# Kernel optimization log

Measured on AMD Instinct MI355X. Metric: run time of the kernel, lower is better.

## Reference

```python
import jax, jax.numpy as jnp
import numpy as np

N = 6144      # total nodes
G = 32        # graphs
NPG = 192     # nodes per graph (N = G*NPG)
FIN = 32      # num_node_features
FE = 8        # num_edge_features
H = 64        # layers = [64, 64]
HM = 128      # layers_MLP = [128]
C = 2         # num_classes
K = 8         # opts.knn
E = 49152     # given edges
EPS = 1e-5


def _bn(x, g, b):
    # BatchNorm1d in train mode: biased batch stats
    m = x.mean(0)
    v = x.var(0)
    return (x - m) * jax.lax.rsqrt(v + EPS) * g + b


def setup_inputs() -> dict:
    key = jax.random.key(0)
    ks = jax.random.split(key, 24)

    def w(k, shape):
        return (jax.random.normal(k, shape, jnp.float32)
                * (1.0 / np.sqrt(shape[0])).astype(np.float32))

    x = jax.random.normal(ks[0], (N, FIN), jnp.float32)
    edge_index = jax.random.randint(ks[1], (2, E), 0, N)
    edge_attr = jax.random.normal(ks[2], (E, FE), jnp.float32)
    batch = jnp.arange(N, dtype=jnp.int64 if jax.config.jax_enable_x64 else jnp.int32) // NPG
    return dict(
        x=x, edge_index=edge_index, edge_attr=edge_attr, batch=batch,
        # EdgeFeatsConv layer 1: mlp(Linear(2*FIN+FE,H), ReLU, Linear(H,H)) + root weight
        ef_w1=w(ks[3], (2 * FIN + FE, H)), ef_b1=jnp.zeros((H,), jnp.float32),
        ef_w2=w(ks[4], (H, H)), ef_b2=jnp.zeros((H,), jnp.float32),
        ef_wroot=w(ks[5], (FIN, H)),
        bn1_g=jnp.ones((H,), jnp.float32), bn1_b=jnp.zeros((H,), jnp.float32),
        # EdgeConv layer 2: mlp(Linear(2*H,H), ReLU, Linear(H,H)), aggr=max
        ec_w1=w(ks[6], (2 * H, H)), ec_b1=jnp.zeros((H,), jnp.float32),
        ec_w2=w(ks[7], (H, H)), ec_b2=jnp.zeros((H,), jnp.float32),
        bn2_g=jnp.ones((H,), jnp.float32), bn2_b=jnp.zeros((H,), jnp.float32),
        # model2: Linear(H,HM), BN, ReLU, Linear(HM,C)
        m2_w1=w(ks[8], (H, HM)), m2_b1=jnp.zeros((HM,), jnp.float32),
        m2_bng=jnp.ones((HM,), jnp.float32), m2_bnb=jnp.zeros((HM,), jnp.float32),
        m2_w2=w(ks[9], (HM, C)), m2_b2=jnp.zeros((C,), jnp.float32),
    )


def reference(x, edge_index, edge_attr, batch,
              ef_w1, ef_b1, ef_w2, ef_b2, ef_wroot, bn1_g, bn1_b,
              ec_w1, ec_b1, ec_w2, ec_b2, bn2_g, bn2_b,
              m2_w1, m2_b1, m2_bng, m2_bnb, m2_w2, m2_b2):
    src, dst = edge_index[0], edge_index[1]

    # ---- layer 1: EdgeFeatsConv (edge-conditioned message MLP + root weight, aggr=sum)
    m = jnp.concatenate([x[dst], x[src], edge_attr], axis=1) @ ef_w1 + ef_b1
    m = jax.nn.relu(m) @ ef_w2 + ef_b2
    x1 = jax.ops.segment_sum(m, dst, num_segments=N) + x @ ef_wroot
    x1 = _bn(x1, bn1_g, bn1_b)

    # ---- layer 2: dynamic KNN graph (loop=False) + to_undirected, then EdgeConv (aggr=max)
    sq = jnp.sum(x1 * x1, axis=1)
    d2 = sq[:, None] + sq[None, :] - 2.0 * (x1 @ x1.T)       # [N, N]
    d2 = d2.at[jnp.arange(N), jnp.arange(N)].set(jnp.inf)    # no self loops
    _, nbr = jax.lax.top_k(-d2, K)                           # [N, K] nearest neighbors
    dst0 = jnp.repeat(jnp.arange(N), K)
    src0 = nbr.reshape(-1)
    s = jnp.concatenate([src0, dst0])                        # undirected (dups OK: max aggr)
    d = jnp.concatenate([dst0, src0])

    h = jnp.concatenate([x1[d], x1[s] - x1[d]], axis=1) @ ec_w1 + ec_b1
    h = jax.nn.relu(h) @ ec_w2 + ec_b2
    x2 = jax.ops.segment_max(h, d, num_segments=N)
    x2 = _bn(x2, bn2_g, bn2_b)

    # ---- per-graph all-pairs |g_i - g_z| (row order: for z, for i)
    g = x2.reshape(G, NPG, H)
    diff = jnp.abs(g[:, None, :, :] - g[:, :, None, :]).reshape(-1, H)  # [G*NPG*NPG, H]

    # ---- model2 MLP + log_softmax
    h2 = jax.nn.relu(_bn(diff @ m2_w1 + m2_b1, m2_bng, m2_bnb))
    out = h2 @ m2_w2 + m2_b2
    return jax.nn.log_softmax(out, axis=1)
```

## Files before the change

### kernel.cpp

```cpp
#include <hip/hip_runtime.h>

#define NN 6144
#define GG 32
#define NPGc 192
#define FINc 32
#define FEc 8
#define Hc 64
#define HMc 128
#define Kc 8
#define Ec 49152
#define NKc (NN*Kc)
#define RTOTc (GG*NPGc*NPGc)

typedef float f32x4 __attribute__((ext_vector_type(4)));
typedef short bf16x8 __attribute__((ext_vector_type(8)));
typedef unsigned long long u64;

__device__ __forceinline__ unsigned short f2bf(float f){
  unsigned u = __float_as_uint(f);
  unsigned r = u + 0x7fffu + ((u>>16)&1u);
  return (unsigned short)(r>>16);
}
__device__ __forceinline__ unsigned fenc(float f){
  unsigned u = __float_as_uint(f);
  return (u & 0x80000000u) ? ~u : (u | 0x80000000u);
}
__device__ __forceinline__ float fdec(unsigned e){
  unsigned u = (e & 0x80000000u) ? (e & 0x7fffffffu) : ~e;
  return __uint_as_float(u);
}
__device__ __forceinline__ void bub8(u64* t8, u64 k){
#pragma unroll
  for (int q=0;q<8;q++){ u64 cur=t8[q]; u64 lo=(k<cur)?k:cur; u64 hi=(k<cur)?cur:k; t8[q]=lo; k=hi; }
}

__global__ void k_init(float* dbins, float* stats){
  int idx = blockIdx.x*256 + threadIdx.x;
  if (idx < 64*256) dbins[idx] = 0.f;
  if (idx < 768) stats[idx] = 0.f;
}

__global__ __launch_bounds__(256) void k_root(const float* __restrict__ x, const float* __restrict__ wr, float* __restrict__ x1a){
  __shared__ float Ws[FINc*Hc];
  __shared__ float xr[4][FINc];
  int t = threadIdx.x;
  for (int q=t;q<FINc*Hc;q+=256) Ws[q] = wr[q];
  int rg = t>>6, j = t&63;
  int r = blockIdx.x*4 + rg;
  if (j < FINc) xr[rg][j] = x[r*FINc + j];
  __syncthreads();
  float a0=0.f, a1=0.f;
#pragma unroll
  for (int k=0;k<FINc;k+=2){
    a0 = fmaf(xr[rg][k],   Ws[k*Hc+j],     a0);
    a1 = fmaf(xr[rg][k+1], Ws[(k+1)*Hc+j], a1);
  }
  x1a[r*Hc + j] = a0 + a1;
}

__global__ __launch_bounds__(256) void k_eac(const float* __restrict__ ea, const float* __restrict__ w1, float* __restrict__ EAc){
  __shared__ float Wc[FEc*Hc];
  int t = threadIdx.x;
  for (int q=t; q<FEc*Hc; q+=256) Wc[q] = w1[64*Hc + q];
  __syncthreads();
  int idx = blockIdx.x*256 + t;
  int e = idx >> 4, c4 = (idx & 15)*4;
  float av[8];
#pragma unroll
  for (int q=0;q<8;q++) av[q] = ea[e*FEc + q];
  float4 o = {0.f,0.f,0.f,0.f};
#pragma unroll
  for (int q=0;q<8;q++){
    o.x = fmaf(av[q], Wc[q*Hc + c4+0], o.x);
    o.y = fmaf(av[q], Wc[q*Hc + c4+1], o.y);
    o.z = fmaf(av[q], Wc[q*Hc + c4+2], o.z);
    o.w = fmaf(av[q], Wc[q*Hc + c4+3], o.w);
  }
  *(float4*)(EAc + (size_t)e*Hc + c4) = o;
}

__global__ __launch_bounds__(256) void k_p12(const float* __restrict__ x, const float* __restrict__ w1, const float* __restrict__ b1,
                                             float* __restrict__ P1, float* __restrict__ P2){
  __shared__ float xs[16][32];
  int t = threadIdx.x;
  int j = t & 63, w = t >> 6;
  float wa[32], wb[32];
#pragma unroll
  for (int k=0;k<32;k++){
    wa[k] = w1[k*Hc + j];
    wb[k] = w1[(32+k)*Hc + j];
  }
  float b1j = b1[j];
  int nb = blockIdx.x * 16;
  for (int q=t; q<16*32; q+=256) xs[q>>5][q&31] = x[(size_t)(nb + (q>>5))*FINc + (q&31)];
  __syncthreads();
#pragma unroll
  for (int it=0; it<4; it++){
    int nl = it*4 + w;
    float a = b1j, b = 0.f;
#pragma unroll
    for (int k=0;k<32;k++){
      float xv = xs[nl][k];
      a = fmaf(xv, wa[k], a);
      b = fmaf(xv, wb[k], b);
    }
    int n = nb + nl;
    P1[(size_t)n*Hc + j] = a;
    P2[(size_t)n*Hc + j] = b;
  }
}

__global__ void k_zero_cnt(unsigned* rcnt){
  int idx = blockIdx.x*256 + threadIdx.x;
  if (idx < NN) rcnt[idx] = 0u;
}
__global__ void k_cnt_dst(const int* __restrict__ ei, unsigned* __restrict__ rcnt){
  int e = blockIdx.x*256 + threadIdx.x;
  atomicAdd(&rcnt[ei[Ec + e]], 1u);
}
__global__ __launch_bounds__(256) void k_scan(const unsigned* __restrict__ rcnt, unsigned* __restrict__ rptr, unsigned* __restrict__ rcur){
  __shared__ unsigned ps[256];
// ... 33 lines not shown
__global__ __launch_bounds__(128) void k_node1(const float* __restrict__ P1, const float* __restrict__ P2, const float* __restrict__ EAc,
        const int* __restrict__ ei, const unsigned* __restrict__ rptr, const unsigned* __restrict__ rlist,
        const float* __restrict__ w2, const float* __restrict__ b2, float* __restrict__ x1a){
  __shared__ __align__(16) float accs[16][68];
  __shared__ __align__(16) float W2T[64][68];
  __shared__ unsigned rp_s[17];
  int t = threadIdx.x;
  int d0 = blockIdx.x * 16;
  for (int q=t; q<64*64; q+=128) W2T[q&63][q>>6] = w2[q];
  if (t < 17) rp_s[t] = rptr[d0 + t];
  __syncthreads();
  int slot = t>>3, cg = t&7, c0 = cg*8;
  int n = d0 + slot;
  float4 p1a = *(const float4*)(P1 + (size_t)n*Hc + c0);
  float4 p1b = *(const float4*)(P1 + (size_t)n*Hc + c0 + 4);
  float acc[8];
#pragma unroll
  for (int q=0;q<8;q++) acc[q] = 0.f;
  unsigned beg = rp_s[slot], end = rp_s[slot+1];
  for (unsigned pos=beg; pos<end; pos++){
    unsigned e = rlist[pos];
    int s = ei[e];
    float4 qa = *(const float4*)(P2 + (size_t)s*Hc + c0);
    float4 qb = *(const float4*)(P2 + (size_t)s*Hc + c0 + 4);
    float4 fa = *(const float4*)(EAc + (size_t)e*Hc + c0);
    float4 fb = *(const float4*)(EAc + (size_t)e*Hc + c0 + 4);
    acc[0] += fmaxf(p1a.x + qa.x + fa.x, 0.f);
    acc[1] += fmaxf(p1a.y + qa.y + fa.y, 0.f);
    acc[2] += fmaxf(p1a.z + qa.z + fa.z, 0.f);
    acc[3] += fmaxf(p1a.w + qa.w + fa.w, 0.f);
    acc[4] += fmaxf(p1b.x + qb.x + fb.x, 0.f);
    acc[5] += fmaxf(p1b.y + qb.y + fb.y, 0.f);
    acc[6] += fmaxf(p1b.z + qb.z + fb.z, 0.f);
    acc[7] += fmaxf(p1b.w + qb.w + fb.w, 0.f);
  }
  *(float4*)&accs[slot][c0]   = make_float4(acc[0],acc[1],acc[2],acc[3]);
  *(float4*)&accs[slot][c0+4] = make_float4(acc[4],acc[5],acc[6],acc[7]);
  __syncthreads();
  float out[8];
#pragma unroll
  for (int q=0;q<8;q++) out[q] = 0.f;
  for (int k4=0;k4<16;k4++){
    float4 hv = *(const float4*)&accs[slot][k4*4];
#pragma unroll
    for (int cc=0;cc<8;cc++){
      float4 wv = *(const float4*)&W2T[c0+cc][k4*4];
      out[cc] = fmaf(hv.x,wv.x, fmaf(hv.y,wv.y, fmaf(hv.z,wv.z, fmaf(hv.w,wv.w, out[cc]))));
    }
  }
  float deg = (float)(end - beg);
  float* px = x1a + (size_t)n*Hc + c0;
#pragma unroll
  for (int cc=0;cc<8;cc++) px[cc] += out[cc] + deg*b2[c0+cc];
}

__global__ __launch_bounds__(256) void k_bn_stats(const float* __restrict__ src, float* __restrict__ gsum, float* __restrict__ gss){
  int t = threadIdx.x;
  int c = t & 63;
  int r0 = blockIdx.x*64 + (t>>6);
  float s=0.f, ss=0.f;
  for (int it=0; it<16; it++){
    int r = r0 + it*4;
    float v = src[r*Hc + c];
    s += v; ss += v*v;
  }
  __shared__ float S[64], SS[64];
  if (t < 64){ S[t]=0.f; SS[t]=0.f; }
  __syncthreads();
  atomicAdd(&S[c], s); atomicAdd(&SS[c], ss);
  __syncthreads();
  if (t < 64){ atomicAdd(&gsum[t], S[t]); atomicAdd(&gss[t], SS[t]); }
}

__global__ void k_bn_fin(const float* gsum, const float* gss, const float* gam, const float* bet, float* sc, float* sh){
  int c = threadIdx.x;
  float mean = gsum[c] / (float)NN;
  float var  = gss[c] / (float)NN - mean*mean;
  float rs = rsqrtf(var + 1e-5f);
  float s = rs * gam[c];
  sc[c] = s; sh[c] = bet[c] - mean*s;
}

__global__ __launch_bounds__(256) void k_apply_bn1_sq(const float* __restrict__ x1a, const float* __restrict__ sc, const float* __restrict__ sh,
                               float* __restrict__ x1bn, float* __restrict__ sqv){
  int t = threadIdx.x;
  int c = t & 63;
  int r = blockIdx.x*4 + (t>>6);
  float v = x1a[r*Hc + c]*sc[c] + sh[c];
  x1bn[r*Hc + c] = v;
  float s = v*v;
#pragma unroll
  for (int off=1; off<64; off<<=1) s += __shfl_xor(s, off, 64);
  if (c == 0) sqv[r] = s;
}

__global__ __launch_bounds__(128,2) void k_knn(const float* __restrict__ x1bn, const float* __restrict__ sqv, u64* __restrict__ parts, int CH){
  __shared__ __align__(16) float XJ[64][68];
  __shared__ float sqj[64];
  int t = threadIdx.x;
  int i1 = blockIdx.x*256 + t;
  int i2 = i1 + 128;
  float4 xa[16], xb[16];
#pragma unroll
  for (int q=0;q<16;q++){
    xa[q] = *(const float4*)(x1bn + (size_t)i1*Hc + q*4);
    xb[q] = *(const float4*)(x1bn + (size_t)i2*Hc + q*4);
  }
  float sqi1 = sqv[i1], sqi2 = sqv[i2];
  u64 t8a[8], t8b[8];
#pragma unroll
  for (int q=0;q<8;q++){ t8a[q] = ~0ull; t8b[q] = ~0ull; }
  float thra = __uint_as_float(0x7f800000u);
  float thrb = thra;
  int cpc = NN / CH;
  int nsub = cpc >> 6;
  int jbase0 = blockIdx.y * cpc;
  for (int sub=0; sub<nsub; sub++){
    int jb = jbase0 + sub*64;
    __syncthreads();
    {
      int c = t>>1, hh = t&1;
      const float4* srcp = (const float4*)(x1bn + (size_t)(jb + c)*Hc + hh*32);
#pragma unroll
      for (int q=0;q<8;q++) *(float4*)&XJ[c][hh*32 + q*4] = srcp[q];
      if (t < 64) sqj[t] = sqv[jb + t];
    }
    __syncthreads();
    for (int j=0;j<64;j++){
      float sqjc = sqj[j];
      float a0=0.f,a1=0.f,a2=0.f,a3=0.f,b0=0.f,b1=0.f,b2=0.f,b3=0.f;
#pragma unroll
      for (int q4=0;q4<4;q4++){
        float4 xj0 = *(const float4*)&XJ[j][q4*16];
        float4 xj1 = *(const float4*)&XJ[j][q4*16+4];
        float4 xj2 = *(const float4*)&XJ[j][q4*16+8];
        float4 xj3 = *(const float4*)&XJ[j][q4*16+12];
        float4 A0 = xa[q4*4+0], A1 = xa[q4*4+1], A2v = xa[q4*4+2], A3 = xa[q4*4+3];
        float4 B0 = xb[q4*4+0], B1 = xb[q4*4+1], B2v = xb[q4*4+2], B3 = xb[q4*4+3];
        a0=fmaf(A0.x,xj0.x,a0); a1=fmaf(A0.y,xj0.y,a1); a2=fmaf(A0.z,xj0.z,a2); a3=fmaf(A0.w,xj0.w,a3);
        b0=fmaf(B0.x,xj0.x,b0); b1=fmaf(B0.y,xj0.y,b1); b2=fmaf(B0.z,xj0.z,b2); b3=fmaf(B0.w,xj0.w,b3);
        a0=fmaf(A1.x,xj1.x,a0); a1=fmaf(A1.y,xj1.y,a1); a2=fmaf(A1.z,xj1.z,a2); a3=fmaf(A1.w,xj1.w,a3);
        b0=fmaf(B1.x,xj1.x,b0); b1=fmaf(B1.y,xj1.y,b1); b2=fmaf(B1.z,xj1.z,b2); b3=fmaf(B1.w,xj1.w,b3);
        a0=fmaf(A2v.x,xj2.x,a0); a1=fmaf(A2v.y,xj2.y,a1); a2=fmaf(A2v.z,xj2.z,a2); a3=fmaf(A2v.w,xj2.w,a3);
        b0=fmaf(B2v.x,xj2.x,b0); b1=fmaf(B2v.y,xj2.y,b1); b2=fmaf(B2v.z,xj2.z,b2); b3=fmaf(B2v.w,xj2.w,b3);
        a0=fmaf(A3.x,xj3.x,a0); a1=fmaf(A3.y,xj3.y,a1); a2=fmaf(A3.z,xj3.z,a2); a3=fmaf(A3.w,xj3.w,a3);
        b0=fmaf(B3.x,xj3.x,b0); b1=fmaf(B3.y,xj3.y,b1); b2=fmaf(B3.z,xj3.z,b2); b3=fmaf(B3.w,xj3.w,b3);
      }
      float dot1 = (a0+a1)+(a2+a3);
      float dot2 = (b0+b1)+(b2+b3);
      int jj = jb + j;
      float d2a = (sqi1 + sqjc) - 2.f*dot1;
      float d2b = (sqi2 + sqjc) - 2.f*dot2;
      bool ia = !(d2a > thra) && (jj != i1);
      bool ib = !(d2b > thrb) && (jj != i2);
      if (__builtin_expect(ia | ib, 0)){
        if (ia){
          u64 ka = (((u64)fenc(d2a))<<32) | (unsigned)jj;
          bub8(t8a, ka);
          thra = fdec((unsigned)(t8a[7]>>32));
        }
        if (ib){
          u64 kb = (((u64)fenc(d2b))<<32) | (unsigned)jj;
          bub8(t8b, kb);
          thrb = fdec((unsigned)(t8b[7]>>32));
        }
      }
    }
  }
  u64* pa = parts + ((size_t)blockIdx.y*NN + i1)*8;
  u64* pb = parts + ((size_t)blockIdx.y*NN + i2)*8;
#pragma unroll
  for (int q=0;q<8;q++){ pa[q] = t8a[q]; pb[q] = t8b[q]; }
}

__global__ __launch_bounds__(256) void k_knn_merge(const u64* __restrict__ parts, int CH, unsigned* __restrict__ nbr){
  int r = blockIdx.x*256 + threadIdx.x;
  u64 t8[8];
#pragma unroll
  for (int q=0;q<8;q++) t8[q] = ~0ull;
  for (int ch=0; ch<CH; ch++){
    const u64* p = parts + ((size_t)ch*NN + r)*8;
    u64 k[8];
#pragma unroll
    for (int q=0;q<8;q++) k[q] = p[q];
#pragma unroll
    for (int q=0;q<8;q++){
      if (k[q] >= t8[7]) break;
      bub8(t8, k[q]);
    }
  }
#pragma unroll
  for (int s=0;s<8;s++) nbr[r*Kc + s] = (unsigned)(t8[s] & 0xffffffffu);
}

__global__ __launch_bounds__(256) void k_pq(const float* __restrict__ x1bn, const float* __restrict__ w1, const float* __restrict__ b1,
                                            float* __restrict__ A2, float* __restrict__ Qm){
  __shared__ float xs[16][64];
  int t = threadIdx.x;
  int j = t & 63, w = t >> 6;
  float wa[64], wb[64];
#pragma unroll
  for (int k=0;k<64;k++){
    float wt  = w1[k*64 + j];
    float wbv = w1[(64+k)*64 + j];
    wa[k] = wt - wbv; wb[k] = wbv;
  }
  float b1j = b1[j];
  int nb = blockIdx.x * 16;
  for (int q=t; q<16*64; q+=256) xs[q>>6][q&63] = x1bn[(size_t)(nb + (q>>6))*64 + (q&63)];
  __syncthreads();
#pragma unroll
  for (int it=0; it<4; it++){
    int nl = it*4 + w;
    float a = b1j, qq = 0.f;
#pragma unroll
    for (int k=0;k<64;k++){
      float xv = xs[nl][k];
      a  = fmaf(xv, wa[k], a);
      qq = fmaf(xv, wb[k], qq);
    }
    int n = nb + nl;
    A2[(size_t)n*64 + j] = a;
    Qm[(size_t)n*64 + j] = qq;
  }
}

__global__ __launch_bounds__(128) void k_edge2max(const float* __restrict__ A2, const float* __restrict__ Qm,
        const unsigned* __restrict__ nbr, const unsigned* __restrict__ rptr, const unsigned* __restrict__ rlist,
        const float* __restrict__ w2, const float* __restrict__ b2, float* __restrict__ x2f){
  __shared__ __align__(16) float W2T[64][68];
  __shared__ __align__(16) float hidT[64][132];
  __shared__ unsigned x2s[17][64];
  __shared__ unsigned rp_s[17];
  __shared__ int wslot[128];
  int t = threadIdx.x;
  int d0 = blockIdx.x * 16;
  for (int q=t; q<64*64; q+=128) W2T[q&63][q>>6] = w2[q];
  for (int q=t; q<17*64; q+=128) ((unsigned*)x2s)[q] = 0x007FFFFFu;
  if (t < 17) rp_s[t] = rptr[d0 + t];
  __syncthreads();
  unsigned rp0 = rp_s[0];
  int total_rev = (int)(rp_s[16] - rp0);
  int eg = t & 15, cg = t >> 4;
  int r0 = eg*8, c0 = cg*8;
  float b2v[8];
#pragma unroll
  for (int cc=0;cc<8;cc++) b2v[cc] = b2[c0+cc];
  int ntile = 1 + ((total_rev + 127) >> 7);
  for (int tile=0; tile<ntile; tile++){
    int d, s, active;
    if (tile == 0){
      d = d0 + (t>>3); s = (int)nbr[(size_t)d*8 + (t&7)]; active = 1; wslot[t] = t>>3;
    } else {
      int idx = (tile-1)*128 + t;
      active = idx < total_rev;
// ... 3 lines not shown
#pragma unroll
        for (int m=1; m<16; m++) sl += (pos >= rp_s[m]) ? 1 : 0;
        s = (int)rlist[pos];
        d = d0 + sl;
        wslot[t] = sl;
      } else { d = d0; s = 0; wslot[t] = 16; }
    }
    if (active){
      const float* pa = A2 + (size_t)d*64;
      const float* pq = Qm + (size_t)s*64;
#pragma unroll
      for (int c4=0; c4<16; c4++){
        float4 va = *(const float4*)(pa + c4*4);
        float4 vq = *(const float4*)(pq + c4*4);
        hidT[c4*4+0][t] = fmaxf(va.x+vq.x, 0.f);
        hidT[c4*4+1][t] = fmaxf(va.y+vq.y, 0.f);
        hidT[c4*4+2][t] = fmaxf(va.z+vq.z, 0.f);
        hidT[c4*4+3][t] = fmaxf(va.w+vq.w, 0.f);
      }
    } else {
#pragma unroll
      for (int c4=0; c4<16; c4++){
        hidT[c4*4+0][t] = 0.f; hidT[c4*4+1][t] = 0.f;
        hidT[c4*4+2][t] = 0.f; hidT[c4*4+3][t] = 0.f;
      }
    }
    __syncthreads();
    float acc[8][8];
#pragma unroll
    for (int i=0;i<8;i++)
#pragma unroll
      for (int cc=0;cc<8;cc++) acc[i][cc] = 0.f;
    for (int k=0;k<64;k+=4){
      float4 wv[8];
#pragma unroll
      for (int cc=0;cc<8;cc++) wv[cc] = *(const float4*)&W2T[c0+cc][k];
#pragma unroll
      for (int kk=0;kk<4;kk++){
        float4 h0 = *(const float4*)&hidT[k+kk][r0];
        float4 h1 = *(const float4*)&hidT[k+kk][r0+4];
        float hh[8] = {h0.x,h0.y,h0.z,h0.w,h1.x,h1.y,h1.z,h1.w};
#pragma unroll
        for (int i=0;i<8;i++)
#pragma unroll
          for (int cc=0;cc<8;cc++)
            acc[i][cc] = fmaf(hh[i], ((const float*)&wv[cc])[kk], acc[i][cc]);
      }
    }
    int cur = wslot[r0];
    float mx[8];
#pragma unroll
    for (int cc=0;cc<8;cc++) mx[cc] = acc[0][cc];
    for (int i=1;i<8;i++){
      int sl = wslot[r0+i];
      if (sl != cur){
#pragma unroll
        for (int cc=0;cc<8;cc++) atomicMax(&x2s[cur][c0+cc], fenc(mx[cc] + b2v[cc]));
        cur = sl;
#pragma unroll
        for (int cc=0;cc<8;cc++) mx[cc] = acc[i][cc];
      } else {
#pragma unroll
        for (int cc=0;cc<8;cc++) mx[cc] = fmaxf(mx[cc], acc[i][cc]);
      }
    }
#pragma unroll
    for (int cc=0;cc<8;cc++) atomicMax(&x2s[cur][c0+cc], fenc(mx[cc] + b2v[cc]));
    __syncthreads();
  }
#pragma unroll
  for (int q=0;q<8;q++){
    int idx = t + q*128;
    int sl = idx >> 6, c = idx & 63;
    x2f[(size_t)(d0+sl)*64 + c] = fdec(x2s[sl][c]);
  }
}

__global__ __launch_bounds__(256) void k_apply_bn2f(const float* __restrict__ x2f, const float* __restrict__ sc, const float* __restrict__ sh, float* __restrict__ x2bn){
  int idx = blockIdx.x*256 + threadIdx.x;
  int c = idx & 63;
  x2bn[idx] = x2f[idx]*sc[c] + sh[c];
}

__global__ __launch_bounds__(256,2) void k_d_stats(const float* __restrict__ x2bn, const float* __restrict__ w1, float* __restrict__ dbins){
  __shared__ __align__(16) char sm[24576 + 16384 + 1024];
  unsigned char* A = (unsigned char*)sm;
  unsigned char* W = (unsigned char*)sm + 24576;
  float* Ssum = (float*)(sm + 40960);
  int t = threadIdx.x;
  int gid = blockIdx.x; int g = gid / NPGc; int z = gid - g*NPGc;
  const float* xg = x2bn + (size_t)g*NPGc*Hc;
  const float* xz = xg + z*Hc;
  Ssum[t] = 0.f;
#pragma unroll
  for (int q=0;q<8;q++){
    int task = t + 256*q; int c = task & 127; int c4 = task >> 7;
    ushort4 p;
    p.x = f2bf(w1[(4*c4+0)*HMc + c]);
    p.y = f2bf(w1[(4*c4+1)*HMc + c]);
    p.z = f2bf(w1[(4*c4+2)*HMc + c]);
    p.w = f2bf(w1[(4*c4+3)*HMc + c]);
    *(ushort4*)(W + c*128 + ((c4*8) ^ ((c&7)<<4))) = p;
  }
#pragma unroll
  for (int q=0;q<12;q++){
    int task = t + 256*q; int i = task >> 4; int c = task & 15;
    float4 a = *(const float4*)(xg + i*Hc + c*4);
    float4 b = *(const float4*)(xz + c*4);
    ushort4 p;
    p.x = f2bf(fabsf(a.x-b.x)); p.y = f2bf(fabsf(a.y-b.y));
    p.z = f2bf(fabsf(a.z-b.z)); p.w = f2bf(fabsf(a.w-b.w));
    *(ushort4*)(A + i*128 + ((c*8) ^ ((i&7)<<4))) = p;
  }
  __syncthreads();
  int w = t>>6, l = t&63, lr = l&15, lg = l>>4;
  int sw = (lr&7)<<4;
  f32x4 zero = {0.f,0.f,0.f,0.f};
  f32x4 acc[3][8];
#pragma unroll
  for (int r=0;r<3;r++)
#pragma unroll
    for (int c=0;c<8;c++) acc[r][c] = zero;
#pragma unroll
  for (int kk=0;kk<2;kk++){
    bf16x8 af[3], bfr[8];
#pragma unroll
    for (int r=0;r<3;r++){
      int row = (w*3+r)*16 + lr;
      af[r] = *(const bf16x8*)(A + row*128 + ((lg*16 + 64*kk) ^ sw));
    }
#pragma unroll
    for (int c=0;c<8;c++){
      int col = c*16 + lr;
      bfr[c] = *(const bf16x8*)(W + col*128 + ((lg*16 + 64*kk) ^ sw));
    }
#pragma unroll
    for (int r=0;r<3;r++)
#pragma unroll
      for (int c=0;c<8;c++)
        acc[r][c] = __builtin_amdgcn_mfma_f32_16x16x32_bf16(af[r], bfr[c], acc[r][c], 0,0,0);
  }
#pragma unroll
  for (int c=0;c<8;c++){
    int col = c*16 + lr;
    float s=0.f, ss=0.f;
#pragma unroll
    for (int r=0;r<3;r++)
#pragma unroll
      for (int q=0;q<4;q++){ float v = acc[r][c][q]; s += v; ss = fmaf(v,v,ss); }
    s  += __shfl_xor(s, 16, 64);  ss += __shfl_xor(ss, 16, 64);
    s  += __shfl_xor(s, 32, 64);  ss += __shfl_xor(ss, 32, 64);
    if (lg == 0){
      atomicAdd(&Ssum[col], s);
      atomicAdd(&Ssum[128+col], ss);
    }
  }
  __syncthreads();
  if (t < 128){
    int bin = gid & 63;
    atomicAdd(&dbins[bin*256 + t], Ssum[t]);
    atomicAdd(&dbins[bin*256 + 128 + t], Ssum[128+t]);
  }
}

__global__ void k_d_fin(const float* __restrict__ dbins, const float* gam, const float* bet, float* dsc, float* dsh){
  int c = threadIdx.x;
  float s=0.f, ss=0.f;
#pragma unroll 8
  for (int b=0;b<64;b++){ s += dbins[b*256 + c]; ss += dbins[b*256 + 128 + c]; }
  float mean = s / (float)RTOTc;
  float var  = ss / (float)RTOTc - mean*mean;
  float rs = rsqrtf(var + 1e-5f);
  float k = rs * gam[c];
  dsc[c] = k; dsh[c] = bet[c] - mean*k;
}

__global__ __launch_bounds__(256,2) void k_d_main(const float* __restrict__ x2bn, const float* __restrict__ w1,
                         const float* __restrict__ w2, const float* __restrict__ b2g,
                         const float* __restrict__ dsc, const float* __restrict__ dsh, float* __restrict__ out){
  __shared__ __align__(16) char sm[49152 + 4096 + 1024];
  unsigned char* A   = (unsigned char*)sm;
  unsigned char* W   = (unsigned char*)sm + 24576;
  unsigned char* W2T = (unsigned char*)sm + 49152;
  float* sS = (float*)(sm + 53248);
  int t = threadIdx.x;
  int gid = blockIdx.x; int g = gid / NPGc; int z = gid - g*NPGc;
  const float* xg = x2bn + (size_t)g*NPGc*Hc;
  const float* xz = xg + z*Hc;
  if (t < 128){ sS[t] = dsc[t]; sS[128+t] = dsh[t]; }
  {
    int c = t>>4, kc = t&15;
    ushort4 p0 = make_ushort4(0,0,0,0), p1 = make_ushort4(0,0,0,0);
    if (c < 2){
      p0.x = f2bf(w2[(kc*8+0)*2 + c]); p0.y = f2bf(w2[(kc*8+1)*2 + c]);
      p0.z = f2bf(w2[(kc*8+2)*2 + c]); p0.w = f2bf(w2[(kc*8+3)*2 + c]);
      p1.x = f2bf(w2[(kc*8+4)*2 + c]); p1.y = f2bf(w2[(kc*8+5)*2 + c]);
      p1.z = f2bf(w2[(kc*8+6)*2 + c]); p1.w = f2bf(w2[(kc*8+7)*2 + c]);
    }
    int byte = c*256 + ((kc*16) ^ ((c&7)<<4));
    *(ushort4*)(W2T + byte) = p0;
    *(ushort4*)(W2T + byte + 8) = p1;
  }
#pragma unroll
  for (int q=0;q<8;q++){
    int task = t + 256*q; int c = task & 127; int c4 = task >> 7;
    ushort4 p;
    p.x = f2bf(w1[(4*c4+0)*HMc + c]);
    p.y = f2bf(w1[(4*c4+1)*HMc + c]);
    p.z = f2bf(w1[(4*c4+2)*HMc + c]);
    p.w = f2bf(w1[(4*c4+3)*HMc + c]);
    *(ushort4*)(W + c*128 + ((c4*8) ^ ((c&7)<<4))) = p;
  }
#pragma unroll
  for (int q=0;q<12;q++){
    int task = t + 256*q; int i = task >> 4; int c = task & 15;
    float4 a = *(const float4*)(xg + i*Hc + c*4);
    float4 b = *(const float4*)(xz + c*4);
    ushort4 p;
    p.x = f2bf(fabsf(a.x-b.x)); p.y = f2bf(fabsf(a.y-b.y));
    p.z = f2bf(fabsf(a.z-b.z)); p.w = f2bf(fabsf(a.w-b.w));
    *(ushort4*)(A + i*128 + ((c*8) ^ ((i&7)<<4))) = p;
  }
  __syncthreads();
  int w = t>>6, l = t&63, lr = l&15, lg = l>>4;
  int sw = (lr&7)<<4;
  f32x4 zero = {0.f,0.f,0.f,0.f};
  f32x4 acc[3][8];
#pragma unroll
  for (int r=0;r<3;r++)
#pragma unroll
    for (int c=0;c<8;c++) acc[r][c] = zero;
#pragma unroll
  for (int kk=0;kk<2;kk++){
    bf16x8 af[3], bfr[8];
#pragma unroll
    for (int r=0;r<3;r++){
      int row = (w*3+r)*16 + lr;
      af[r] = *(const bf16x8*)(A + row*128 + ((lg*16 + 64*kk) ^ sw));
    }
#pragma unroll
    for (int c=0;c<8;c++){
      int col = c*16 + lr;
      bfr[c] = *(const bf16x8*)(W + col*128 + ((lg*16 + 64*kk) ^ sw));
    }
#pragma unroll
    for (int r=0;r<3;r++)
#pragma unroll
      for (int c=0;c<8;c++)
        acc[r][c] = __builtin_amdgcn_mfma_f32_16x16x32_bf16(af[r], bfr[c], acc[r][c], 0,0,0);
  }
  __syncthreads();
#pragma unroll
  for (int r=0;r<3;r++){
#pragma unroll
    for (int c=0;c<8;c++){
      int col = c*16 + lr;
      float scl = sS[col], shf = sS[128+col];
#pragma unroll
      for (int q=0;q<4;q++){
        int row = (w*3+r)*16 + lg*4 + q;
        float v = fmaxf(acc[r][c][q]*scl + shf, 0.f);
        *(unsigned short*)(A + row*256 + ((col*2) ^ ((row&7)<<4))) = f2bf(v);
      }
    }
  }
  __syncthreads();
  f32x4 acc2[3];
#pragma unroll
  for (int r=0;r<3;r++) acc2[r] = zero;
#pragma unroll
  for (int kk=0;kk<4;kk++){
    bf16x8 bw = *(const bf16x8*)(W2T + lr*256 + ((lg*16 + 64*kk) ^ sw));
#pragma unroll
    for (int r=0;r<3;r++){
      int row = (w*3+r)*16 + lr;
      bf16x8 ah = *(const bf16x8*)(A + row*256 + ((lg*16 + 64*kk) ^ sw));
      acc2[r] = __builtin_amdgcn_mfma_f32_16x16x32_bf16(ah, bw, acc2[r], 0,0,0);
    }
  }
  float b2a = b2g[0], b2b = b2g[1];
  size_t obase = (size_t)gid * NPGc;
#pragma unroll
  for (int r=0;r<3;r++){
#pragma unroll
    for (int q=0;q<4;q++){
      float o = acc2[r][q];
      float oo = __shfl_xor(o, 1, 64);
      if (lr < 2){
        int row = (w*3+r)*16 + lg*4 + q;
        float self = o + ((lr==0) ? b2a : b2b);
        float oth  = oo + ((lr==0) ? b2b : b2a);
        float mx = fmaxf(self, oth);
        float lse = mx + logf(expf(self-mx) + expf(oth-mx));
        out[(obase + row)*2 + lr] = self - lse;
      }
    }
  }
}

extern "C" void kernel_launch(void* const* d_in, const int* in_sizes, int n_in,
                              void* d_out, int out_size, void* d_ws, size_t ws_size,
                              hipStream_t stream){
  const float* x    = (const float*)d_in[0];
  const int*   ei   = (const int*)d_in[1];
  const float* ea   = (const float*)d_in[2];
  const float* efw1 = (const float*)d_in[4];
  const float* efb1 = (const float*)d_in[5];
  const float* efw2 = (const float*)d_in[6];
  const float* efb2 = (const float*)d_in[7];
  const float* efwr = (const float*)d_in[8];
  const float* bn1g = (const float*)d_in[9];
  const float* bn1b = (const float*)d_in[10];
  const float* ecw1 = (const float*)d_in[11];
  const float* ecb1 = (const float*)d_in[12];
  const float* ecw2 = (const float*)d_in[13];
  const float* ecb2 = (const float*)d_in[14];
  const float* bn2g = (const float*)d_in[15];
  const float* bn2b = (const float*)d_in[16];
  const float* m2w1 = (const float*)d_in[17];
  const float* m2bng = (const float*)d_in[19];
  const float* m2bnb = (const float*)d_in[20];
  const float* m2w2  = (const float*)d_in[21];
  const float* m2b2  = (const float*)d_in[22];

  char* ws = (char*)d_ws;
  float*    x1a   = (float*)(ws + 0);
  float*    x1bn  = (float*)(ws + 1572864);
  float*    x2bn  = (float*)(ws + 3145728);
  float*    x2f   = (float*)(ws + 4718592);
  float*    sqv   = (float*)(ws + 6291456);
  unsigned* nbr   = (unsigned*)(ws + 6316032);
  float*    stats = (float*)(ws + 6512640);
  float*    dbins = (float*)(ws + 6515712);
  u64*      parts = (u64*)(ws + 6581248);
  float*    A2    = (float*)(ws + 0);
  float*    Qm    = (float*)(ws + 3145728);
  float*    P1    = (float*)(ws + 3145728);
  float*    P2    = (float*)(ws + 4718592);
  unsigned* rcnt  = (unsigned*)(ws + 6581248);
  unsigned* rptr  = rcnt + 6400;
  unsigned* rcur  = rptr + 6400;
  unsigned* rlist = rcur + 6400;
  float*    EAc   = (float*)(ws + 6581248 + 4194304);
  float *g1sum = stats,     *g1ss = stats+64,  *sc1 = stats+128, *sh1 = stats+192;
  float *g2sum = stats+256, *g2ss = stats+320, *sc2 = stats+384, *sh2 = stats+448;
  float *dsc = stats+512, *dsh = stats+640;
  float* outp = (float*)d_out;

  int CH = 96;
  if (ws_size < 6581248ull + (size_t)NN*96*64) CH = 48;
  if (ws_size < 6581248ull + (size_t)NN*48*64) CH = 24;

  k_init<<<64,256,0,stream>>>(dbins, stats);
  k_root<<<1536,256,0,stream>>>(x, efwr, x1a);
  k_eac<<<3072,256,0,stream>>>(ea, efw1, EAc);
  k_zero_cnt<<<24,256,0,stream>>>(rcnt);
  k_cnt_dst<<<192,256,0,stream>>>(ei, rcnt);
  k_scan<<<1,256,0,stream>>>(rcnt, rptr, rcur);
  k_fill_dst<<<192,256,0,stream>>>(ei, rcur, rlist);
  k_p12<<<384,256,0,stream>>>(x, efw1, efb1, P1, P2);
  k_node1<<<384,128,0,stream>>>(P1, P2, EAc, ei, rptr, rlist, efw2, efb2, x1a);
  k_bn_stats<<<96,256,0,stream>>>(x1a, g1sum, g1ss);
  k_bn_fin<<<1,64,0,stream>>>(g1sum, g1ss, bn1g, bn1b, sc1, sh1);
  k_apply_bn1_sq<<<1536,256,0,stream>>>(x1a, sc1, sh1, x1bn, sqv);
  dim3 kg(24, CH);
  k_knn<<<kg,128,0,stream>>>(x1bn, sqv, parts, CH);
  k_knn_merge<<<24,256,0,stream>>>(parts, CH, nbr);
  k_zero_cnt<<<24,256,0,stream>>>(rcnt);
  k_rev_cnt<<<192,256,0,stream>>>(nbr, rcnt);
  k_scan<<<1,256,0,stream>>>(rcnt, rptr, rcur);
  k_rev_fill<<<192,256,0,stream>>>(nbr, rcur, rlist);
  k_pq<<<384,256,0,stream>>>(x1bn, ecw1, ecb1, A2, Qm);
  k_edge2max<<<384,128,0,stream>>>(A2, Qm, nbr, rptr, rlist, ecw2, ecb2, x2f);
  k_bn_stats<<<96,256,0,stream>>>(x2f, g2sum, g2ss);
  k_bn_fin<<<1,64,0,stream>>>(g2sum, g2ss, bn2g, bn2b, sc2, sh2);
  k_apply_bn2f<<<1536,256,0,stream>>>(x2f, sc2, sh2, x2bn);
  k_d_stats<<<6144,256,0,stream>>>(x2bn, m2w1, dbins);
  k_d_fin<<<1,128,0,stream>>>(dbins, m2bng, m2bnb, dsc, dsh);
  k_d_main<<<6144,256,0,stream>>>(x2bn, m2w1, m2w2, m2b2, dsc, dsh, outp);
}
```

Baseline: 554.1 us.

## Compute KNN distances with bf16x3 split MFMA instead of scalar FP32 FMAs

Replaces the scalar FP32 pairwise-dot KNN kernel with a tiled MFMA kernel. Each feature is split into three bf16 terms (hi, lo, lo2), and six cross-product pairs are laid out along a 384-wide K dimension to approximate FP32 dot products on matrix cores. Distances are staged through LDS for the per-row top-8 bubble insert. The workspace layout is changed to hold the expanded operands, and the column-chunk count is reworked. The split-bf16 precision could reorder near-tie neighbors.

```diff
diff --git a/kernel.cpp b/kernel.cpp
--- a/kernel.cpp
+++ b/kernel.cpp
@@ -11,6 +11,7 @@
 #define Ec 49152
 #define NKc (NN*Kc)
 #define RTOTc (GG*NPGc*NPGc)
+#define KEc 384
 
 typedef float f32x4 __attribute__((ext_vector_type(4)));
 typedef short bf16x8 __attribute__((ext_vector_type(8)));
@@ -236,95 +237,132 @@
 }
 
 __global__ __launch_bounds__(256) void k_apply_bn1_sq(const float* __restrict__ x1a, const float* __restrict__ sc, const float* __restrict__ sh,
-                               float* __restrict__ x1bn, float* __restrict__ sqv){
+                               float* __restrict__ x1bn, float* __restrict__ sqv,
+                               unsigned short* __restrict__ XAe, unsigned short* __restrict__ XBe){
   int t = threadIdx.x;
   int c = t & 63;
   int r = blockIdx.x*4 + (t>>6);
   float v = x1a[r*Hc + c]*sc[c] + sh[c];
   x1bn[r*Hc + c] = v;
+  unsigned short hu = f2bf(v);
+  float hf = __uint_as_float(((unsigned)hu)<<16);
+  float r1 = v - hf;
+  unsigned short lu = f2bf(r1);
+  float lf = __uint_as_float(((unsigned)lu)<<16);
+  unsigned short l2u = f2bf(r1 - lf);
+  size_t base = (size_t)r*KEc + c;
+  XAe[base      ] = hu;  XAe[base+ 64] = lu;  XAe[base+128] = l2u;
+  XAe[base+192] = hu;   XAe[base+256] = lu;  XAe[base+320] = hu;
+  XBe[base      ] = hu;  XBe[base+ 64] = hu;  XBe[base+128] = hu;
+  XBe[base+192] = lu;   XBe[base+256] = lu;  XBe[base+320] = l2u;
   float s = v*v;
 #pragma unroll
   for (int off=1; off<64; off<<=1) s += __shfl_xor(s, off, 64);
   if (c == 0) sqv[r] = s;
 }
 
-__global__ __launch_bounds__(128,2) void k_knn(const float* __restrict__ x1bn, const float* __restrict__ sqv, u64* __restrict__ parts, int CH){
-  __shared__ __align__(16) float XJ[64][68];
-  __shared__ float sqj[64];
-  int t = threadIdx.x;
-  int i1 = blockIdx.x*256 + t;
-  int i2 = i1 + 128;
-  float4 xa[16], xb[16];
-#pragma unroll
-  for (int q=0;q<16;q++){
-    xa[q] = *(const float4*)(x1bn + (size_t)i1*Hc + q*4);
-    xb[q] = *(const float4*)(x1bn + (size_t)i2*Hc + q*4);
-  }
-  float sqi1 = sqv[i1], sqi2 = sqv[i2];
-  u64 t8a[8], t8b[8];
-#pragma unroll
-  for (int q=0;q<8;q++){ t8a[q] = ~0ull; t8b[q] = ~0ull; }
-  float thra = __uint_as_float(0x7f800000u);
-  float thrb = thra;
-  int cpc = NN / CH;
-  int nsub = cpc >> 6;
-  int jbase0 = blockIdx.y * cpc;
-  for (int sub=0; sub<nsub; sub++){
-    int jb = jbase0 + sub*64;
-    __syncthreads();
-    {
-      int c = t>>1, hh = t&1;
-      const float4* srcp = (const float4*)(x1bn + (size_t)(jb + c)*Hc + hh*32);
-#pragma unroll
-      for (int q=0;q<8;q++) *(float4*)&XJ[c][hh*32 + q*4] = srcp[q];
-      if (t < 64) sqj[t] = sqv[jb + t];
-    }
-    __syncthreads();
-    for (int j=0;j<64;j++){
-      float sqjc = sqj[j];
-      float a0=0.f,a1=0.f,a2=0.f,a3=0.f,b0=0.f,b1=0.f,b2=0.f,b3=0.f;
-#pragma unroll
-      for (int q4=0;q4<4;q4++){
-        float4 xj0 = *(const float4*)&XJ[j][q4*16];
-        float4 xj1 = *(const float4*)&XJ[j][q4*16+4];
-        float4 xj2 = *(const float4*)&XJ[j][q4*16+8];
-        float4 xj3 = *(const float4*)&XJ[j][q4*16+12];
-        float4 A0 = xa[q4*4+0], A1 = xa[q4*4+1], A2v = xa[q4*4+2], A3 = xa[q4*4+3];
-        float4 B0 = xb[q4*4+0], B1 = xb[q4*4+1], B2v = xb[q4*4+2], B3 = xb[q4*4+3];
-        a0=fmaf(A0.x,xj0.x,a0); a1=fmaf(A0.y,xj0.y,a1); a2=fmaf(A0.z,xj0.z,a2); a3=fmaf(A0.w,xj0.w,a3);
-        b0=fmaf(B0.x,xj0.x,b0); b1=fmaf(B0.y,xj0.y,b1); b2=fmaf(B0.z,xj0.z,b2); b3=fmaf(B0.w,xj0.w,b3);
-        a0=fmaf(A1.x,xj1.x,a0); a1=fmaf(A1.y,xj1.y,a1); a2=fmaf(A1.z,xj1.z,a2); a3=fmaf(A1.w,xj1.w,a3);
-        b0=fmaf(B1.x,xj1.x,b0); b1=fmaf(B1.y,xj1.y,b1); b2=fmaf(B1.z,xj1.z,b2); b3=fmaf(B1.w,xj1.w,b3);
-        a0=fmaf(A2v.x,xj2.x,a0); a1=fmaf(A2v.y,xj2.y,a1); a2=fmaf(A2v.z,xj2.z,a2); a3=fmaf(A2v.w,xj2.w,a3);
-        b0=fmaf(B2v.x,xj2.x,b0); b1=fmaf(B2v.y,xj2.y,b1); b2=fmaf(B2v.z,xj2.z,b2); b3=fmaf(B2v.w,xj2.w,b3);
-        a0=fmaf(A3.x,xj3.x,a0); a1=fmaf(A3.y,xj3.y,a1); a2=fmaf(A3.z,xj3.z,a2); a3=fmaf(A3.w,xj3.w,a3);
-        b0=fmaf(B3.x,xj3.x,b0); b1=fmaf(B3.y,xj3.y,b1); b2=fmaf(B3.z,xj3.z,b2); b3=fmaf(B3.w,xj3.w,b3);
-      }
-      float dot1 = (a0+a1)+(a2+a3);
-      float dot2 = (b0+b1)+(b2+b3);
-      int jj = jb + j;
-      float d2a = (sqi1 + sqjc) - 2.f*dot1;
-      float d2b = (sqi2 + sqjc) - 2.f*dot2;
-      bool ia = !(d2a > thra) && (jj != i1);
-      bool ib = !(d2b > thrb) && (jj != i2);
-      if (__builtin_expect(ia | ib, 0)){
-        if (ia){
-          u64 ka = (((u64)fenc(d2a))<<32) | (unsigned)jj;
-          bub8(t8a, ka);
-          thra = fdec((unsigned)(t8a[7]>>32));
+__global__ __launch_bounds__(256,2) void k_knn2(const unsigned short* __restrict__ XAe, const unsigned short* __restrict__ XBe,
+        const float* __restrict__ sqv, u64* __restrict__ parts, int NT){
+  __shared__ __align__(16) char lds[50688];
+  unsigned char* Abuf = (unsigned char*)lds;
+  unsigned char* Bbuf = (unsigned char*)lds + 32768;
+  float* d2buf = (float*)lds;
+  float* sqi = (float*)(lds + 49152);
+  float* sqj = (float*)(lds + 50176);
+  int t = threadIdx.x;
+  int bx = blockIdx.x;
+  int irow = bx*256 + t;
+  sqi[t] = sqv[irow];
+  u64 t8[8];
+#pragma unroll
+  for (int q=0;q<8;q++) t8[q] = ~0ull;
+  float thr = __uint_as_float(0x7f800000u);
+  int w = t>>6, l = t&63, lr = l&15, lg = l>>4;
+  int wr = w>>1, wc = w&1;
+  int sw = (lr&7)<<4;
+  f32x4 zero = {0.f,0.f,0.f,0.f};
+  for (int jt=0; jt<NT; jt++){
+    int jbase = (blockIdx.y*NT + jt)*128;
+    if (t < 128) sqj[t] = sqv[jbase + t];
+    f32x4 acc[8][4];
+#pragma unroll
+    for (int rg=0;rg<8;rg++)
+#pragma unroll
+      for (int cg=0;cg<4;cg++) acc[rg][cg] = zero;
+    for (int ks=0; ks<6; ks++){
+      __syncthreads();
+#pragma unroll
+      for (int q=0;q<8;q++){
+        int task = t + 256*q; int r = task>>3, s = task&7;
+        bf16x8 v = *(const bf16x8*)(XAe + (size_t)(bx*256+r)*KEc + ks*64 + s*8);
+        *(bf16x8*)(Abuf + r*128 + ((s*16) ^ ((r&7)<<4))) = v;
+      }
+#pragma unroll
+      for (int q=0;q<4;q++){
+        int task = t + 256*q; int r = task>>3, s = task&7;
+        bf16x8 v = *(const bf16x8*)(XBe + (size_t)(jbase+r)*KEc + ks*64 + s*8);
+        *(bf16x8*)(Bbuf + r*128 + ((s*16) ^ ((r&7)<<4))) = v;
+      }
+      __syncthreads();
+#pragma unroll
+      for (int kk=0;kk<2;kk++){
+        bf16x8 af[8], bfr[4];
+#pragma unroll
+        for (int rg=0;rg<8;rg++){
+          int row = wr*128 + rg*16 + lr;
+          af[rg] = *(const bf16x8*)(Abuf + row*128 + ((lg*16 + 64*kk) ^ sw));
         }
-        if (ib){
-          u64 kb = (((u64)fenc(d2b))<<32) | (unsigned)jj;
-          bub8(t8b, kb);
-          thrb = fdec((unsigned)(t8b[7]>>32));
+#pragma unroll
+        for (int cg=0;cg<4;cg++){
+          int col = wc*64 + cg*16 + lr;
+          bfr[cg] = *(const bf16x8*)(Bbuf + col*128 + ((lg*16 + 64*kk) ^ sw));
         }
-      }
-    }
-  }
-  u64* pa = parts + ((size_t)blockIdx.y*NN + i1)*8;
-  u64* pb = parts + ((size_t)blockIdx.y*NN + i2)*8;
-#pragma unroll
-  for (int q=0;q<8;q++){ pa[q] = t8a[q]; pb[q] = t8b[q]; }
+#pragma unroll
+        for (int rg=0;rg<8;rg++)
+#pragma unroll
+          for (int cg=0;cg<4;cg++)
+            acc[rg][cg] = __builtin_amdgcn_mfma_f32_16x16x32_bf16(af[rg], bfr[cg], acc[rg][cg], 0,0,0);
+      }
+    }
+#pragma unroll
+    for (int rnd=0; rnd<4; rnd++){
+      __syncthreads();
+      if (wc == (rnd>>1)){
+#pragma unroll
+        for (int cg2=0; cg2<2; cg2++){
+          int cg = (rnd&1)*2 + cg2;
+          int col_local = wc*64 + cg*16 + lr;
+          int col_r = col_local - rnd*32;
+          float sj = sqj[col_local];
+#pragma unroll
+          for (int rg=0;rg<8;rg++){
+            int rb = wr*128 + rg*16 + lg*4;
+            float4 s4 = *(const float4*)&sqi[rb];
+            f32x4 a = acc[rg][cg];
+            d2buf[(rb+0)*33 + col_r] = (s4.x + sj) - 2.f*a[0];
+            d2buf[(rb+1)*33 + col_r] = (s4.y + sj) - 2.f*a[1];
+            d2buf[(rb+2)*33 + col_r] = (s4.z + sj) - 2.f*a[2];
+            d2buf[(rb+3)*33 + col_r] = (s4.w + sj) - 2.f*a[3];
+          }
+        }
+      }
+      __syncthreads();
+      int jg0 = jbase + rnd*32;
+      const float* drow = d2buf + t*33;
+      for (int c=0;c<32;c++){
+        float d2 = drow[c];
+        int jj = jg0 + c;
+        if (__builtin_expect(!(d2 > thr) && (jj != irow), 0)){
+          u64 k = (((u64)fenc(d2))<<32) | (unsigned)jj;
+          bub8(t8, k);
+          thr = fdec((unsigned)(t8[7]>>32));
+        }
+      }
+    }
+  }
+  u64* pa = parts + ((size_t)blockIdx.y*NN + irow)*8;
+#pragma unroll
+  for (int q=0;q<8;q++) pa[q] = t8[q];
 }
 
 __global__ __launch_bounds__(256) void k_knn_merge(const u64* __restrict__ parts, int CH, unsigned* __restrict__ nbr){
@@ -744,24 +782,27 @@
   unsigned* nbr   = (unsigned*)(ws + 6316032);
   float*    stats = (float*)(ws + 6512640);
   float*    dbins = (float*)(ws + 6515712);
-  u64*      parts = (u64*)(ws + 6581248);
+  unsigned* rcnt  = (unsigned*)(ws + 6581248);
+  unsigned* rptr  = rcnt + 6400;
+  unsigned* rcur  = rptr + 6400;
+  unsigned* rlist = rcur + 6400;
+  unsigned short* XAe = (unsigned short*)(ws + 6974464);
+  unsigned short* XBe = (unsigned short*)(ws + 11693056);
+  u64*      parts = (u64*)(ws + 16411648);
   float*    A2    = (float*)(ws + 0);
   float*    Qm    = (float*)(ws + 3145728);
   float*    P1    = (float*)(ws + 3145728);
   float*    P2    = (float*)(ws + 4718592);
-  unsigned* rcnt  = (unsigned*)(ws + 6581248);
-  unsigned* rptr  = rcnt + 6400;
-  unsigned* rcur  = rptr + 6400;
-  unsigned* rlist = rcur + 6400;
-  float*    EAc   = (float*)(ws + 6581248 + 4194304);
+  float*    EAc   = (float*)(ws + 11693056);
   float *g1sum = stats,     *g1ss = stats+64,  *sc1 = stats+128, *sh1 = stats+192;
   float *g2sum = stats+256, *g2ss = stats+320, *sc2 = stats+384, *sh2 = stats+448;
   float *dsc = stats+512, *dsh = stats+640;
   float* outp = (float*)d_out;
 
-  int CH = 96;
-  if (ws_size < 6581248ull + (size_t)NN*96*64) CH = 48;
-  if (ws_size < 6581248ull + (size_t)NN*48*64) CH = 24;
+  int NT = 1;
+  if (ws_size < 16411648ull + 48ull*NN*64) NT = 2;
+  if (ws_size < 16411648ull + 24ull*NN*64) NT = 4;
+  int CH = 48/NT;
 
   k_init<<<64,256,0,stream>>>(dbins, stats);
   k_root<<<1536,256,0,stream>>>(x, efwr, x1a);
@@ -774,9 +815,9 @@
   k_node1<<<384,128,0,stream>>>(P1, P2, EAc, ei, rptr, rlist, efw2, efb2, x1a);
   k_bn_stats<<<96,256,0,stream>>>(x1a, g1sum, g1ss);
   k_bn_fin<<<1,64,0,stream>>>(g1sum, g1ss, bn1g, bn1b, sc1, sh1);
-  k_apply_bn1_sq<<<1536,256,0,stream>>>(x1a, sc1, sh1, x1bn, sqv);
-  dim3 kg(24, CH);
-  k_knn<<<kg,128,0,stream>>>(x1bn, sqv, parts, CH);
+  k_apply_bn1_sq<<<1536,256,0,stream>>>(x1a, sc1, sh1, x1bn, sqv, XAe, XBe);
+  dim3 kg(24, 48/NT);
+  k_knn2<<<kg,256,0,stream>>>(XAe, XBe, sqv, parts, NT);
   k_knn_merge<<<24,256,0,stream>>>(parts, CH, nbr);
   k_zero_cnt<<<24,256,0,stream>>>(rcnt);
   k_rev_cnt<<<192,256,0,stream>>>(nbr, rcnt);
```

Measured after the change: 547.9 us. About the same (-1.1%).

## Compute MLP batch-norm statistics via Gram matrix of diff features instead of full GEMM

Applied to the files above, without the earlier changes.

Replaces the stats pass, which ran the full 1.18M x 64 x 128 GEMM only to get per-column sum and sum of squares, with an algebraic form. The new pass accumulates the 64x64 second-moment matrix D^T D and the column sums of D, then derives the mean and variance of D@W1 as W^T S and w^T M w. This shrinks the stats GEMM output width from 128 to 64 columns and drops the W1 staging. In exchange it adds partial buffers, a reduction kernel and a serial finalize kernel, and only 256 blocks run the main pass.

```diff
diff --git a/kernel.cpp b/kernel.cpp
--- a/kernel.cpp
+++ b/kernel.cpp
@@ -34,9 +34,8 @@
   for (int q=0;q<8;q++){ u64 cur=t8[q]; u64 lo=(k<cur)?k:cur; u64 hi=(k<cur)?cur:k; t8[q]=lo; k=hi; }
 }
 
-__global__ void k_init(float* dbins, float* stats){
+__global__ void k_init(float* stats){
   int idx = blockIdx.x*256 + threadIdx.x;
-  if (idx < 64*256) dbins[idx] = 0.f;
   if (idx < 768) stats[idx] = 0.f;
 }
 
@@ -494,97 +493,108 @@
   x2bn[idx] = x2f[idx]*sc[c] + sh[c];
 }
 
-__global__ __launch_bounds__(256,2) void k_d_stats(const float* __restrict__ x2bn, const float* __restrict__ w1, float* __restrict__ dbins){
-  __shared__ __align__(16) char sm[24576 + 16384 + 1024];
-  unsigned char* A = (unsigned char*)sm;
-  unsigned char* W = (unsigned char*)sm + 24576;
-  float* Ssum = (float*)(sm + 40960);
-  int t = threadIdx.x;
-  int gid = blockIdx.x; int g = gid / NPGc; int z = gid - g*NPGc;
+__global__ __launch_bounds__(256) void k_d_M(const float* __restrict__ x2bn, float* __restrict__ Mpart, float* __restrict__ Spart){
+  __shared__ __align__(16) float xgs[192*64];
+  __shared__ __align__(16) unsigned short Gs[64*200];
+  int t = threadIdx.x;
+  int g = blockIdx.x >> 3, zc = blockIdx.x & 7;
   const float* xg = x2bn + (size_t)g*NPGc*Hc;
-  const float* xz = xg + z*Hc;
-  Ssum[t] = 0.f;
-#pragma unroll
-  for (int q=0;q<8;q++){
-    int task = t + 256*q; int c = task & 127; int c4 = task >> 7;
-    ushort4 p;
-    p.x = f2bf(w1[(4*c4+0)*HMc + c]);
-    p.y = f2bf(w1[(4*c4+1)*HMc + c]);
-    p.z = f2bf(w1[(4*c4+2)*HMc + c]);
-    p.w = f2bf(w1[(4*c4+3)*HMc + c]);
-    *(ushort4*)(W + c*128 + ((c4*8) ^ ((c&7)<<4))) = p;
-  }
-#pragma unroll
-  for (int q=0;q<12;q++){
-    int task = t + 256*q; int i = task >> 4; int c = task & 15;
-    float4 a = *(const float4*)(xg + i*Hc + c*4);
-    float4 b = *(const float4*)(xz + c*4);
-    ushort4 p;
-    p.x = f2bf(fabsf(a.x-b.x)); p.y = f2bf(fabsf(a.y-b.y));
-    p.z = f2bf(fabsf(a.z-b.z)); p.w = f2bf(fabsf(a.w-b.w));
-    *(ushort4*)(A + i*128 + ((c*8) ^ ((i&7)<<4))) = p;
-  }
-  __syncthreads();
+  for (int q=t; q<3072; q+=256)
+    *(float4*)&xgs[q*4] = *(const float4*)(xg + (size_t)q*4);
   int w = t>>6, l = t&63, lr = l&15, lg = l>>4;
-  int sw = (lr&7)<<4;
+  int wr = w>>1, wc = w&1;
   f32x4 zero = {0.f,0.f,0.f,0.f};
-  f32x4 acc[3][8];
-#pragma unroll
-  for (int r=0;r<3;r++)
-#pragma unroll
-    for (int c=0;c<8;c++) acc[r][c] = zero;
-#pragma unroll
-  for (int kk=0;kk<2;kk++){
-    bf16x8 af[3], bfr[8];
-#pragma unroll
-    for (int r=0;r<3;r++){
-      int row = (w*3+r)*16 + lr;
-      af[r] = *(const bf16x8*)(A + row*128 + ((lg*16 + 64*kk) ^ sw));
-    }
-#pragma unroll
-    for (int c=0;c<8;c++){
-      int col = c*16 + lr;
-      bfr[c] = *(const bf16x8*)(W + col*128 + ((lg*16 + 64*kk) ^ sw));
-    }
-#pragma unroll
-    for (int r=0;r<3;r++)
-#pragma unroll
-      for (int c=0;c<8;c++)
-        acc[r][c] = __builtin_amdgcn_mfma_f32_16x16x32_bf16(af[r], bfr[c], acc[r][c], 0,0,0);
-  }
-#pragma unroll
-  for (int c=0;c<8;c++){
-    int col = c*16 + lr;
-    float s=0.f, ss=0.f;
-#pragma unroll
-    for (int r=0;r<3;r++)
-#pragma unroll
-      for (int q=0;q<4;q++){ float v = acc[r][c][q]; s += v; ss = fmaf(v,v,ss); }
-    s  += __shfl_xor(s, 16, 64);  ss += __shfl_xor(ss, 16, 64);
-    s  += __shfl_xor(s, 32, 64);  ss += __shfl_xor(ss, 32, 64);
-    if (lg == 0){
-      atomicAdd(&Ssum[col], s);
-      atomicAdd(&Ssum[128+col], ss);
-    }
-  }
-  __syncthreads();
-  if (t < 128){
-    int bin = gid & 63;
-    atomicAdd(&dbins[bin*256 + t], Ssum[t]);
-    atomicAdd(&dbins[bin*256 + 128 + t], Ssum[128+t]);
-  }
-}
-
-__global__ void k_d_fin(const float* __restrict__ dbins, const float* gam, const float* bet, float* dsc, float* dsh){
+  f32x4 acc[2][2];
+  acc[0][0]=zero; acc[0][1]=zero; acc[1][0]=zero; acc[1][1]=zero;
+  float sloc = 0.f;
+  for (int zi=0; zi<24; zi++){
+    int z = zc*24 + zi;
+    __syncthreads();
+#pragma unroll
+    for (int q=0;q<48;q++){
+      int elem = t + 256*q;
+      int i = elem >> 6, k = elem & 63;
+      float d = fabsf(xgs[i*64 + k] - xgs[z*64 + k]);
+      unsigned short hv = f2bf(d);
+      sloc += __uint_as_float(((unsigned)hv)<<16);
+      Gs[k*200 + i] = hv;
+    }
+    __syncthreads();
+#pragma unroll
+    for (int ks=0; ks<6; ks++){
+      bf16x8 af[2], bg[2];
+#pragma unroll
+      for (int mi=0;mi<2;mi++){
+        int row = wr*32 + mi*16 + lr;
+        af[mi] = *(const bf16x8*)(Gs + row*200 + ks*32 + lg*8);
+      }
+#pragma unroll
+      for (int ni=0;ni<2;ni++){
+        int col = wc*32 + ni*16 + lr;
+        bg[ni] = *(const bf16x8*)(Gs + col*200 + ks*32 + lg*8);
+      }
+#pragma unroll
+      for (int mi=0;mi<2;mi++)
+#pragma unroll
+        for (int ni=0;ni<2;ni++)
+          acc[mi][ni] = __builtin_amdgcn_mfma_f32_16x16x32_bf16(af[mi], bg[ni], acc[mi][ni], 0,0,0);
+    }
+  }
+  float* mp = Mpart + (size_t)blockIdx.x*4096;
+#pragma unroll
+  for (int mi=0;mi<2;mi++)
+#pragma unroll
+    for (int ni=0;ni<2;ni++)
+#pragma unroll
+      for (int q=0;q<4;q++){
+        int Mrow = wr*32 + mi*16 + lg*4 + q;
+        int Mcol = wc*32 + ni*16 + lr;
+        mp[Mrow*64 + Mcol] = acc[mi][ni][q];
+      }
+  __syncthreads();
+  xgs[t] = sloc;
+  __syncthreads();
+  if (t < 64) Spart[(size_t)blockIdx.x*64 + t] = (xgs[t] + xgs[64+t]) + (xgs[128+t] + xgs[192+t]);
+}
+
+__global__ __launch_bounds__(256) void k_d_red(const float* __restrict__ Mpart, const float* __restrict__ Spart,
+                                               float* __restrict__ Msum, float* __restrict__ Ssum){
+  int b = blockIdx.x, t = threadIdx.x;
+  if (b < 16){
+    int e = b*256 + t;
+    float s = 0.f;
+    for (int p=0;p<256;p++) s += Mpart[(size_t)p*4096 + e];
+    Msum[e] = s;
+  } else if (t < 64){
+    float s = 0.f;
+    for (int p=0;p<256;p++) s += Spart[(size_t)p*64 + t];
+    Ssum[t] = s;
+  }
+}
+
+__global__ void k_d_fin2(const float* __restrict__ Msum, const float* __restrict__ Ssum, const float* __restrict__ w1,
+                         const float* gam, const float* bet, float* dsc, float* dsh){
   int c = threadIdx.x;
-  float s=0.f, ss=0.f;
+  float wv[64];
+#pragma unroll
+  for (int k=0;k<64;k++) wv[k] = w1[k*HMc + c];
+  float mean = 0.f;
 #pragma unroll 8
-  for (int b=0;b<64;b++){ s += dbins[b*256 + c]; ss += dbins[b*256 + 128 + c]; }
-  float mean = s / (float)RTOTc;
-  float var  = ss / (float)RTOTc - mean*mean;
+  for (int k=0;k<64;k++) mean = fmaf(Ssum[k], wv[k], mean);
+  mean /= (float)RTOTc;
+  float msq = 0.f;
+  for (int k=0;k<64;k++){
+    const float* Mr = Msum + k*64;
+    float mk = 0.f;
+#pragma unroll 8
+    for (int ll=0;ll<64;ll++) mk = fmaf(Mr[ll], wv[ll], mk);
+    msq = fmaf(wv[k], mk, msq);
+  }
+  msq /= (float)RTOTc;
+  float var = msq - mean*mean;
   float rs = rsqrtf(var + 1e-5f);
-  float k = rs * gam[c];
-  dsc[c] = k; dsh[c] = bet[c] - mean*k;
+  float kk = rs * gam[c];
+  dsc[c] = kk; dsh[c] = bet[c] - mean*kk;
 }
 
 __global__ __launch_bounds__(256,2) void k_d_main(const float* __restrict__ x2bn, const float* __restrict__ w1,
@@ -743,27 +753,30 @@
   float*    sqv   = (float*)(ws + 6291456);
   unsigned* nbr   = (unsigned*)(ws + 6316032);
   float*    stats = (float*)(ws + 6512640);
-  float*    dbins = (float*)(ws + 6515712);
-  u64*      parts = (u64*)(ws + 6581248);
+  unsigned* rcnt  = (unsigned*)(ws + 6581248);
+  unsigned* rptr  = rcnt + 6400;
+  unsigned* rcur  = rptr + 6400;
+  unsigned* rlist = rcur + 6400;
+  u64*      parts = (u64*)(ws + 6974464);
+  float*    EAc   = (float*)(ws + 6974464);
+  float*    Mpart = (float*)(ws + 6974464);
+  float*    Spart = (float*)(ws + 6974464 + 4194304);
+  float*    Msum  = (float*)(ws + 6974464 + 4259840);
+  float*    Ssum  = (float*)(ws + 6974464 + 4276224);
   float*    A2    = (float*)(ws + 0);
   float*    Qm    = (float*)(ws + 3145728);
   float*    P1    = (float*)(ws + 3145728);
   float*    P2    = (float*)(ws + 4718592);
-  unsigned* rcnt  = (unsigned*)(ws + 6581248);
-  unsigned* rptr  = rcnt + 6400;
-  unsigned* rcur  = rptr + 6400;
-  unsigned* rlist = rcur + 6400;
-  float*    EAc   = (float*)(ws + 6581248 + 4194304);
   float *g1sum = stats,     *g1ss = stats+64,  *sc1 = stats+128, *sh1 = stats+192;
   float *g2sum = stats+256, *g2ss = stats+320, *sc2 = stats+384, *sh2 = stats+448;
   float *dsc = stats+512, *dsh = stats+640;
   float* outp = (float*)d_out;
 
   int CH = 96;
-  if (ws_size < 6581248ull + (size_t)NN*96*64) CH = 48;
-  if (ws_size < 6581248ull + (size_t)NN*48*64) CH = 24;
-
-  k_init<<<64,256,0,stream>>>(dbins, stats);
+  if (ws_size < 6974464ull + (size_t)NN*96*64) CH = 48;
+  if (ws_size < 6974464ull + (size_t)NN*48*64) CH = 24;
+
+  k_init<<<3,256,0,stream>>>(stats);
   k_root<<<1536,256,0,stream>>>(x, efwr, x1a);
   k_eac<<<3072,256,0,stream>>>(ea, efw1, EAc);
   k_zero_cnt<<<24,256,0,stream>>>(rcnt);
@@ -787,7 +800,8 @@
   k_bn_stats<<<96,256,0,stream>>>(x2f, g2sum, g2ss);
   k_bn_fin<<<1,64,0,stream>>>(g2sum, g2ss, bn2g, bn2b, sc2, sh2);
   k_apply_bn2f<<<1536,256,0,stream>>>(x2f, sc2, sh2, x2bn);
-  k_d_stats<<<6144,256,0,stream>>>(x2bn, m2w1, dbins);
-  k_d_fin<<<1,128,0,stream>>>(dbins, m2bng, m2bnb, dsc, dsh);
+  k_d_M<<<256,256,0,stream>>>(x2bn, Mpart, Spart);
+  k_d_red<<<17,256,0,stream>>>(Mpart, Spart, Msum, Ssum);
+  k_d_fin2<<<1,128,0,stream>>>(Msum, Ssum, m2w1, m2bng, m2bnb, dsc, dsh);
   k_d_main<<<6144,256,0,stream>>>(x2bn, m2w1, m2w2, m2b2, dsc, dsh, outp);
 }
```

Measured after the change: 662.5 us. 1.2x slower.
